# Kernel optimization log

Hardware: AMD Instinct MI355X
Metric: run time of the kernel (lower is better)

Reference implementation:

```python
import jax, jax.numpy as jnp
import numpy as np

N = 500_000          # number of particles
D = 6                # phase-space dimension
N_BINS = 128         # bins per axis
SQRT2 = 1.4142135623730951
BANDWIDTH = 1.0      # kernel width relative to bin width (module default)


def setup_inputs() -> dict:
    key = jax.random.key(0)
    x = jax.random.normal(key, (N, D), dtype=jnp.float32)
    edges = jnp.linspace(-3.0, 3.0, N_BINS + 1, dtype=jnp.float32)
    return {"x": x, "bin_edges_x": edges, "bin_edges_y": edges}


def _cdf_weights(u, edges, bw):
    """Per-point Gaussian mass in each bin via CDF (erf) differences.

    u: (n,), edges: (m+1,) -> weights (n, m); row sums <= 1.
    """
    z = jax.scipy.special.erf((edges[None, :] - u[:, None]) / (bw * SQRT2))  # (n, m+1)
    return 0.5 * (z[:, 1:] - z[:, :-1])  # (n, m)


def reference(x, bin_edges_x, bin_edges_y):
    dx = bin_edges_x[1] - bin_edges_x[0]
    dy = bin_edges_y[1] - bin_edges_y[0]
    bw_x = BANDWIDTH * dx
    bw_y = BANDWIDTH * dy
    # axis = (0, 1): project onto first two phase-space coordinates
    wx = _cdf_weights(x[:, 0], bin_edges_x, bw_x)  # (n, bx)
    wy = _cdf_weights(x[:, 1], bin_edges_y, bw_y)  # (n, by)
    hist = jnp.einsum('ni,nj->ij', wx, wy)         # (bx, by)
    # normalize to a probability density over the grid
    hist = hist / (hist.sum() * dx * dy)
    return hist
```

## Files before the change

### kernel.cpp

```cpp
#include <hip/hip_runtime.h>
#include <math.h>


#define NBINS   128
#define NB2     (NBINS * NBINS)
#define KC      128
#define AXB     16384
#define BUFB    (2 * AXB)
#define THREADS 512
#define NBLOCKS 512
#define QSCALE  320.0f

typedef int i32x4 __attribute__((ext_vector_type(4)));

static __device__ __forceinline__ unsigned short f2bf(float f) {
    unsigned int b = __float_as_uint(f);
    b += 0x7fff + ((b >> 16) & 1);
    return (unsigned short)(b >> 16);
}
static __device__ __forceinline__ float bf2f(unsigned short u) {
    return __uint_as_float((unsigned int)u << 16);
}

static __device__ __forceinline__ float erf_fast(float x) {
    const float ax = fabsf(x);
    const float t  = __builtin_amdgcn_rcpf(fmaf(0.3275911f, ax, 1.0f));
    const float e  = __expf(-x * x);
    float p = fmaf(1.061405429f, t, -1.453152027f);
    p = fmaf(p, t, 1.421413741f);
    p = fmaf(p, t, -0.284496736f);
    p = fmaf(p, t, 0.254829592f);
    p = p * t;
    return copysignf(fmaf(-p, e, 1.0f), x);
}

__global__ __launch_bounds__(THREADS, 4) void hist_mfma_kernel(
    const float* __restrict__ x,
    const float* __restrict__ edges_x,
    const float* __restrict__ edges_y,
    unsigned short* __restrict__ partials,
    float* __restrict__ btot,
    int n)
{
    __shared__ __align__(16) signed char sh[2 * BUFB];
    __shared__ int xw[8];

    const int tid  = threadIdx.x;
    const int lane = tid & 63;
    const int wv   = tid >> 6;

    const float e0x = edges_x[0];
    const float dxw = edges_x[1] - e0x;
    const float e0y = edges_y[0];
    const float dyw = edges_y[1] - e0y;

    const int a  = tid >> 8;
    const int pl = (tid & 255) >> 1;
    const int h  = tid & 1;
    const float e0   = a ? e0y : e0x;
    const float invd = 1.0f / (a ? dyw : dxw);
    const float cc   = 0.7071067811865476f;
    signed char* const sbase =
        sh + a * AXB + (pl >> 6) * 1024 + ((pl >> 4) & 3) * 256 + (pl & 15);

    i32x4 acc[4][4];
    #pragma unroll
    for (int i = 0; i < 4; ++i)
        #pragma unroll
        for (int j = 0; j < 4; ++j)
            acc[i][j] = (i32x4){0, 0, 0, 0};

    const int rowQ = ((wv >> 1) & 1) * 4;
    const int colQ = (wv & 1) * 4;
    const int ks   = wv >> 2;
    const signed char* const rbase = sh + ks * 1024 + lane * 16;

    const int nchunks = (n + KC - 1) / KC;

    auto loadu = [&](int c) -> float {
        if (c < nchunks) {
            const int p = c * KC + pl;
            if (p < n) return x[(size_t)p * 6 + a];
        }
        return 1e30f;
    };
    int b0; signed char qv[4];
    auto calc = [&](float u) {
        const float spos = (u - e0) * invd;
        int b = (int)floorf(spos + 0.5f) - 4;
        b0 = b < 0 ? 0 : (b > NBINS - 8 ? NBINS - 8 : b);
        const float t0 = ((float)(b0 + 4 * h) - spos) * cc;
        float z[5];
        #pragma unroll
        for (int k = 0; k < 5; ++k) z[k] = erf_fast(t0 + (float)k * cc);
        #pragma unroll
        for (int k = 0; k < 4; ++k)
            qv[k] = (signed char)(int)rintf(0.5f * (z[k + 1] - z[k]) * QSCALE);
    };
    auto scat = [&](int Woff, int b0old) {
        #pragma unroll
        for (int k = 0; k < 4; ++k) {
            const int b = b0old + 4 * h + k;
            sbase[Woff + (b >> 4) * 2048 + (b & 15) * 16] = 0;
        }
        #pragma unroll
        for (int k = 0; k < 4; ++k) {
            const int b = b0 + 4 * h + k;
            sbase[Woff + (b >> 4) * 2048 + (b & 15) * 16] = qv[k];
        }
    };
    auto mstep = [&](int Roff) {
        i32x4 av[4], bv[4];
        #pragma unroll
        for (int i = 0; i < 4; ++i)
            av[i] = *(const i32x4*)(rbase + Roff + (rowQ + i) * 2048);
        #pragma unroll
        for (int j = 0; j < 4; ++j)
            bv[j] = *(const i32x4*)(rbase + Roff + AXB + (colQ + j) * 2048);
        #pragma unroll
        for (int i = 0; i < 4; ++i)
            #pragma unroll
            for (int j = 0; j < 4; ++j)
                acc[i][j] = __builtin_amdgcn_mfma_i32_16x16x64_i8(
                    av[i], bv[j], acc[i][j], 0, 0, 0);
    };

    float4* zp = (float4*)sh;
    #pragma unroll
    for (int i = 0; i < 8; ++i)
        zp[tid + i * THREADS] = (float4){0.f, 0.f, 0.f, 0.f};

    int c = blockIdx.x;
    float u1 = loadu(c + NBLOCKS);
    calc(loadu(c));
    int b0A = 0, b0B = 0;
    __syncthreads();
    scat(0, b0A); b0A = b0;
    __syncthreads();

    while (true) {
        {
            const float u2 = loadu(c + 2 * NBLOCKS);
            calc(u1);
            scat(BUFB, b0B); b0B = b0;
            mstep(0);
            __syncthreads();
            c += NBLOCKS; u1 = u2;
            if (c >= nchunks) break;
        }
        {
            const float u2 = loadu(c + 2 * NBLOCKS);
            calc(u1);
            scat(0, b0A); b0A = b0;
            mstep(BUFB);
            __syncthreads();
            c += NBLOCKS; u1 = u2;
            if (c >= nchunks) break;
        }
    }

    if (wv >= 4) {
        int* dst = (int*)sh + (wv - 4) * 4096;
        #pragma unroll
        for (int i = 0; i < 4; ++i)
            #pragma unroll
            for (int j = 0; j < 4; ++j)
                #pragma unroll
                for (int g = 0; g < 4; ++g)
                    dst[((i * 4 + j) * 4 + g) * 64 + lane] = acc[i][j][g];
    }
    __syncthreads();

    int bsum = 0;
    if (wv < 4) {
        const float qs = 1.0f / (QSCALE * QSCALE);
        const int* src = (const int*)sh + wv * 4096;
        unsigned short* my = partials + (size_t)blockIdx.x * NB2;
        const int r0 = (lane >> 4) * 4;
        const int c0 = lane & 15;
        #pragma unroll
        for (int i = 0; i < 4; ++i)
            #pragma unroll
            for (int j = 0; j < 4; ++j)
                #pragma unroll
                for (int g = 0; g < 4; ++g) {
                    const int v = acc[i][j][g] + src[((i * 4 + j) * 4 + g) * 64 + lane];
                    bsum += v;
                    const int row = (rowQ + i) * 16 + r0 + g;
                    const int col = (colQ + j) * 16 + c0;
                    my[row * NBINS + col] = f2bf((float)v * qs);
                }
    }
    #pragma unroll
    for (int off = 32; off > 0; off >>= 1) bsum += __shfl_down(bsum, off, 64);
    if (lane == 0) xw[wv] = bsum;
    __syncthreads();
    if (tid == 0) {
        const float qs = 1.0f / (QSCALE * QSCALE);
        btot[blockIdx.x] = (float)(xw[0] + xw[1] + xw[2] + xw[3]) * qs;
    }
}

__global__ void reduce_kernel(const unsigned short* __restrict__ partials,
                              const float* __restrict__ btot,
                              const float* __restrict__ edges_x,
                              const float* __restrict__ edges_y,
                              float* __restrict__ out)
{
    __shared__ float4 red[8][32];
    __shared__ float ws[4];
    __shared__ float stot;

    const int t = threadIdx.x;
    const int bin4 = t & 31;
    const int pg = t >> 5;
    const int binBase = blockIdx.x * 128;

    float tl = btot[t] + btot[t + 256];
    #pragma unroll
    for (int off = 32; off > 0; off >>= 1) tl += __shfl_down(tl, off, 64);
    if ((t & 63) == 0) ws[t >> 6] = tl;

    const unsigned short* p =
        partials + (size_t)(pg * 64) * NB2 + binBase + bin4 * 4;
    float4 s = {0.f, 0.f, 0.f, 0.f};
    #pragma unroll 8
    for (int k = 0; k < 64; ++k) {
        const ushort4 v = *(const ushort4*)(p + (size_t)k * NB2);
        s.x += bf2f(v.x); s.y += bf2f(v.y); s.z += bf2f(v.z); s.w += bf2f(v.w);
    }
    red[pg][bin4] = s;
    __syncthreads();

    if (t == 0) {
        const float dxw = edges_x[1] - edges_x[0];
        const float dyw = edges_y[1] - edges_y[0];
        stot = 1.0f / ((ws[0] + ws[1] + ws[2] + ws[3]) * dxw * dyw);
    }
    __syncthreads();

    if (t < 32) {
        float4 aa = red[0][t];
        #pragma unroll
        for (int g = 1; g < 8; ++g) {
            const float4 b = red[g][t];
            aa.x += b.x; aa.y += b.y; aa.z += b.z; aa.w += b.w;
        }
        aa.x *= stot; aa.y *= stot; aa.z *= stot; aa.w *= stot;
        *(float4*)(out + binBase + t * 4) = aa;
    }
}

extern "C" void kernel_launch(void* const* d_in, const int* in_sizes, int n_in,
                              void* d_out, int out_size, void* d_ws, size_t ws_size,
                              hipStream_t stream)
{
    const float* x  = (const float*)d_in[0];
    const float* ex = (const float*)d_in[1];
    const float* ey = (const float*)d_in[2];
    float* out = (float*)d_out;
    const int n = in_sizes[0] / 6;

    unsigned short* partials = (unsigned short*)d_ws;
    float* btot = (float*)((char*)d_ws + (size_t)NBLOCKS * NB2 * 2);

    hist_mfma_kernel<<<NBLOCKS, THREADS, 0, stream>>>(x, ex, ey, partials, btot, n);
    reduce_kernel<<<NB2 / 128, 256, 0, stream>>>(partials, btot, ex, ey, out);
}
```

Measured before the change: 86.37 us.

## Fuse final reduction into histogram kernel via grid-wide flag barrier

Removes the separate reduce kernel launch. Each block publishes its partial histogram and a magic flag, spins until all 512 blocks have published, then reduces a 32-bin slice across all partials. This saves one launch and the gap between kernels, but it relies on all blocks being co-resident. Flags are never reset, so stale magic values from an earlier call could let blocks read partials before they are updated.

Result: slower. 163.8 us (+89.6%).

```diff
diff --git a/kernel.cpp b/kernel.cpp
--- a/kernel.cpp
+++ b/kernel.cpp
@@ -10,6 +10,7 @@
 #define THREADS 512
 #define NBLOCKS 512
 #define QSCALE  320.0f
+#define FLAG_MAGIC 0x5A17C0DE
 
 typedef int i32x4 __attribute__((ext_vector_type(4)));
 
@@ -34,16 +35,20 @@
     return copysignf(fmaf(-p, e, 1.0f), x);
 }
 
-__global__ __launch_bounds__(THREADS, 4) void hist_mfma_kernel(
+__global__ __launch_bounds__(THREADS, 4) void hist_fused_kernel(
     const float* __restrict__ x,
     const float* __restrict__ edges_x,
     const float* __restrict__ edges_y,
     unsigned short* __restrict__ partials,
     float* __restrict__ btot,
+    int* __restrict__ flags,
+    float* __restrict__ out,
     int n)
 {
     __shared__ __align__(16) signed char sh[2 * BUFB];
     __shared__ int xw[8];
+    __shared__ float xwf[8];
+    __shared__ float snorm;
 
     const int tid  = threadIdx.x;
     const int lane = tid & 63;
@@ -198,56 +203,55 @@
     if (tid == 0) {
         const float qs = 1.0f / (QSCALE * QSCALE);
         btot[blockIdx.x] = (float)(xw[0] + xw[1] + xw[2] + xw[3]) * qs;
-    }
-}
-
-__global__ void reduce_kernel(const unsigned short* __restrict__ partials,
-                              const float* __restrict__ btot,
-                              const float* __restrict__ edges_x,
-                              const float* __restrict__ edges_y,
-                              float* __restrict__ out)
-{
-    __shared__ float4 red[8][32];
-    __shared__ float ws[4];
-    __shared__ float stot;
-
-    const int t = threadIdx.x;
-    const int bin4 = t & 31;
-    const int pg = t >> 5;
-    const int binBase = blockIdx.x * 128;
-
-    float tl = btot[t] + btot[t + 256];
+        __threadfence();
+        __hip_atomic_store(&flags[blockIdx.x], FLAG_MAGIC,
+                           __ATOMIC_RELAXED, __HIP_MEMORY_SCOPE_AGENT);
+    }
+
+    {
+        volatile int spun = 0;
+        while (__hip_atomic_load(&flags[tid], __ATOMIC_RELAXED,
+                                 __HIP_MEMORY_SCOPE_AGENT) != FLAG_MAGIC) {
+            __builtin_amdgcn_s_sleep(8);
+            (void)spun;
+        }
+    }
+    __syncthreads();
+    __threadfence();
+
+    const int kg  = tid >> 5;
+    const int bin = tid & 31;
+    const int binBase = blockIdx.x * 32;
+
+    float tl = btot[tid];
     #pragma unroll
     for (int off = 32; off > 0; off >>= 1) tl += __shfl_down(tl, off, 64);
-    if ((t & 63) == 0) ws[t >> 6] = tl;
-
-    const unsigned short* p =
-        partials + (size_t)(pg * 64) * NB2 + binBase + bin4 * 4;
-    float4 s = {0.f, 0.f, 0.f, 0.f};
+    if (lane == 0) xwf[wv] = tl;
+
+    const unsigned short* p = partials + (size_t)(kg * 32) * NB2 + binBase + bin;
+    float s = 0.0f;
     #pragma unroll 8
-    for (int k = 0; k < 64; ++k) {
-        const ushort4 v = *(const ushort4*)(p + (size_t)k * NB2);
-        s.x += bf2f(v.x); s.y += bf2f(v.y); s.z += bf2f(v.z); s.w += bf2f(v.w);
-    }
-    red[pg][bin4] = s;
-    __syncthreads();
-
-    if (t == 0) {
-        const float dxw = edges_x[1] - edges_x[0];
-        const float dyw = edges_y[1] - edges_y[0];
-        stot = 1.0f / ((ws[0] + ws[1] + ws[2] + ws[3]) * dxw * dyw);
-    }
-    __syncthreads();
-
-    if (t < 32) {
-        float4 aa = red[0][t];
-        #pragma unroll
-        for (int g = 1; g < 8; ++g) {
-            const float4 b = red[g][t];
-            aa.x += b.x; aa.y += b.y; aa.z += b.z; aa.w += b.w;
-        }
-        aa.x *= stot; aa.y *= stot; aa.z *= stot; aa.w *= stot;
-        *(float4*)(out + binBase + t * 4) = aa;
+    for (int k = 0; k < 32; ++k)
+        s += bf2f(p[(size_t)k * NB2]);
+
+    __syncthreads();
+    float* red = (float*)sh;
+    red[kg * 32 + bin] = s;
+    __syncthreads();
+
+    if (tid == 0) {
+        float tot = 0.0f;
+        #pragma unroll
+        for (int w = 0; w < 8; ++w) tot += xwf[w];
+        snorm = 1.0f / (tot * dxw * dyw);
+    }
+    __syncthreads();
+
+    if (tid < 32) {
+        float acc2 = 0.0f;
+        #pragma unroll
+        for (int g = 0; g < 16; ++g) acc2 += red[g * 32 + tid];
+        out[binBase + tid] = acc2 * snorm;
     }
 }
 
@@ -262,8 +266,9 @@
     const int n = in_sizes[0] / 6;
 
     unsigned short* partials = (unsigned short*)d_ws;
-    float* btot = (float*)((char*)d_ws + (size_t)NBLOCKS * NB2 * 2);
-
-    hist_mfma_kernel<<<NBLOCKS, THREADS, 0, stream>>>(x, ex, ey, partials, btot, n);
-    reduce_kernel<<<NB2 / 128, 256, 0, stream>>>(partials, btot, ex, ey, out);
-}
+    float* btot  = (float*)((char*)d_ws + (size_t)NBLOCKS * NB2 * 2);
+    int*   flags = (int*)(btot + NBLOCKS);
+
+    hist_fused_kernel<<<NBLOCKS, THREADS, 0, stream>>>(
+        x, ex, ey, partials, btot, flags, out, n);
+}
```
